# Kernel optimization log

Measured on AMD Instinct MI355X. Metric: run time of the kernel, lower is better.

Reference implementation:

```python
import jax, jax.numpy as jnp
import numpy as np

D_IN = 1024
D_OUT = 1024
NUM_HEADS = 16
HEAD_DIM = D_OUT // NUM_HEADS


def setup_inputs() -> dict:
    key = jax.random.key(0)
    ks = jax.random.split(key, 6)
    s = 0.02
    return {
        "x": jax.random.normal(ks[0], (2, 2048, D_IN), dtype=jnp.float32),
        "Wq": jax.random.normal(ks[1], (D_IN, D_OUT), dtype=jnp.float32) * s,
        "Wk": jax.random.normal(ks[2], (D_IN, D_OUT), dtype=jnp.float32) * s,
        "Wv": jax.random.normal(ks[3], (D_IN, D_OUT), dtype=jnp.float32) * s,
        "Wo": jax.random.normal(ks[4], (D_OUT, D_OUT), dtype=jnp.float32) * s,
        "bo": jax.random.normal(ks[5], (D_OUT,), dtype=jnp.float32) * s,
    }


def reference(x, Wq, Wk, Wv, Wo, bo):
    B, S, d_in = x.shape
    # projections, split into heads: [B, H, S, Dh]
    def split_heads(t):
        return t.reshape(B, S, NUM_HEADS, HEAD_DIM).transpose(0, 2, 1, 3)

    q = split_heads(x @ Wq)
    k = split_heads(x @ Wk)
    v = split_heads(x @ Wv)

    # raw scores [B, H, S, S]
    scores = jnp.einsum("bhqd,bhkd->bhqk", q, k)
    # causal mask applied BEFORE scaling (as in original; -inf unaffected by scale)
    causal = jnp.triu(jnp.ones((S, S), dtype=bool), k=1)
    scores = jnp.where(causal, -jnp.inf, scores)
    # NOTE: original scales by sqrt(d_in) = sqrt(x.shape[-1]), not sqrt(head_dim)
    scores = scores / jnp.sqrt(jnp.asarray(d_in, dtype=scores.dtype))
    weights = jax.nn.softmax(scores, axis=-1)
    # dropout p=0.0 -> identity

    out = jnp.einsum("bhqk,bhkd->bhqd", weights, v)
    out = out.transpose(0, 2, 1, 3).reshape(B, S, D_OUT)
    return out @ Wo + bo
```

## Files before the change

### kernel.cpp

```cpp
#include <hip/hip_runtime.h>

#define D_MODEL 1024
#define SEQ     2048
#define BATCH   2
#define NHEAD   16
#define HDIM    64

typedef __attribute__((ext_vector_type(4))) float  f32x4;
typedef __attribute__((ext_vector_type(8))) __bf16 bf16x8;
typedef __attribute__((ext_vector_type(4))) __bf16 bf16x4;
typedef __attribute__((ext_vector_type(2))) unsigned int u32x2;

__device__ __forceinline__ void gld_lds16(const void* g, void* l) {
  __builtin_amdgcn_global_load_lds(
      (const __attribute__((address_space(1))) void*)g,
      (__attribute__((address_space(3))) void*)l, 16, 0, 0);
}

__global__ void k_convert(const float* __restrict__ in, __bf16* __restrict__ out) {
  int i = blockIdx.x * blockDim.x + threadIdx.x;
  float4 v = ((const float4*)in)[i];
  bf16x4 o;
  o[0] = (__bf16)v.x; o[1] = (__bf16)v.y; o[2] = (__bf16)v.z; o[3] = (__bf16)v.w;
  ((bf16x4*)out)[i] = o;
}

__global__ void k_transw(const float* __restrict__ Wq, const float* __restrict__ Wk,
                         const float* __restrict__ Wv, const float* __restrict__ Wo,
                         __bf16* __restrict__ Wqkvt, __bf16* __restrict__ Wot) {
  __shared__ __bf16 T[64][72];
  const int z = blockIdx.z;
  const float* src = (z==0)?Wq:(z==1)?Wk:(z==2)?Wv:Wo;
  __bf16* dst = (z<3) ? (Wqkvt + (size_t)z*D_MODEL*D_MODEL) : Wot;
  const float scl = (z==0) ? 0.03125f : 1.0f;
  const int k0 = blockIdx.x*64, n0 = blockIdx.y*64;
  const int t = threadIdx.x;
  const int kl = t>>4, nl4 = (t&15)*4;
  #pragma unroll
  for (int part = 0; part < 4; ++part) {
    const int k = part*16 + kl;
    float4 v = *(const float4*)(src + (size_t)(k0+k)*D_MODEL + n0 + nl4);
    T[nl4+0][k] = (__bf16)(v.x*scl);
    T[nl4+1][k] = (__bf16)(v.y*scl);
    T[nl4+2][k] = (__bf16)(v.z*scl);
    T[nl4+3][k] = (__bf16)(v.w*scl);
  }
  __syncthreads();
  const int nl = t>>3, kc = (t&7)*8;
  #pragma unroll
  for (int part = 0; part < 2; ++part) {
    int n = part*32 + nl;
    bf16x8 o = *(const bf16x8*)&T[n][kc];
    *(bf16x8*)(dst + (size_t)(n0+n)*D_MODEL + k0 + kc) = o;
  }
}

template<int OUTF32>
__global__ __launch_bounds__(256)
void k_gemm_bt(const __bf16* __restrict__ A, const __bf16* __restrict__ Bt,
               void* __restrict__ Cv, const float* __restrict__ bias,
               const int K, const int N) {
  __shared__ __bf16 As[128*32];
  __shared__ __bf16 Bs[128*32];
  const int t = threadIdx.x;
  const int w = t>>6, l = t&63;
  const int lr = l&15, g = l>>4;
  const int m0 = blockIdx.y*128, n0 = blockIdx.x*128;
  const int wr = (w>>1)*64, wc = (w&1)*64;
  f32x4 acc[4][4] = {};

  const int srow = w*16 + (l>>2);
  const int sc8  = (l&3)*8;
  const __bf16* Ag = A  + (size_t)(m0 + srow)*K + sc8;
  const __bf16* Bg = Bt + (size_t)(n0 + srow)*K + sc8;
  char* Al = (char*)As + w*1024;
  char* Bl = (char*)Bs + w*1024;

  for (int k0 = 0; k0 < K; k0 += 32) {
    __syncthreads();
    gld_lds16(Ag + k0,                 Al);
    gld_lds16(Ag + (size_t)64*K + k0,  Al + 4096);
    gld_lds16(Bg + k0,                 Bl);
    gld_lds16(Bg + (size_t)64*K + k0,  Bl + 4096);
    __syncthreads();
    bf16x8 af[4], bf[4];
    #pragma unroll
    for (int mi=0;mi<4;++mi)
      af[mi] = *(const bf16x8*)((const char*)As + (wr + mi*16 + lr)*64 + (g<<4));
    #pragma unroll
    for (int ni=0;ni<4;++ni)
      bf[ni] = *(const bf16x8*)((const char*)Bs + (wc + ni*16 + lr)*64 + (g<<4));
    #pragma unroll
    for (int mi=0;mi<4;++mi)
      #pragma unroll
      for (int ni=0;ni<4;++ni)
        acc[mi][ni] = __builtin_amdgcn_mfma_f32_16x16x32_bf16(af[mi], bf[ni], acc[mi][ni], 0, 0, 0);
  }

  if (OUTF32) {
    float* C = (float*)Cv;
    #pragma unroll
    for (int ni=0;ni<4;++ni) {
      const int col = n0 + wc + ni*16 + lr;
      const float bv = bias[col];
      #pragma unroll
      for (int mi=0;mi<4;++mi)
        #pragma unroll
        for (int r=0;r<4;++r) {
          const int row = m0 + wr + mi*16 + g*4 + r;
          C[(size_t)row*N + col] = acc[mi][ni][r] + bv;
        }
    }
  } else {
    __bf16* C = (__bf16*)Cv;
    #pragma unroll
    for (int ni=0;ni<4;++ni) {
      const int col = n0 + wc + ni*16 + lr;
      #pragma unroll
      for (int mi=0;mi<4;++mi)
        #pragma unroll
        for (int r=0;r<4;++r) {
          const int row = m0 + wr + mi*16 + g*4 + r;
          C[(size_t)row*N + col] = (__bf16)acc[mi][ni][r];
        }
    }
  }
}

__global__ __launch_bounds__(256)
void k_attn(const __bf16* __restrict__ QKV, __bf16* __restrict__ AO) {
  __shared__ __bf16 Ks[2][64*64];
  __shared__ __bf16 Vs[2][64*64];
  const int t = threadIdx.x;
  const int w = t>>6, l = t&63;
  const int lr = l&15, g = l>>4;
  const int bh = blockIdx.y, b = bh>>4, h = bh&15;
  const size_t rb = (size_t)b*SEQ;

  const int skey = t>>3, sc = t&7;
  const __bf16* Kg = QKV + rb*3072 + 1024 + h*64 + sc*8;
  const __bf16* Vg = Kg + 1024;
  const int ksw = skey*128 + ((sc ^ (skey&7))<<4);
  const int vsw = ((skey>>4)*4 + (sc>>1))*512 + (skey&15)*32 + (sc&1)*16;

  for (int half = 0; half < 2; ++half) {
    const int qb = (half==0) ? (int)blockIdx.x : 31 - (int)blockIdx.x;
    const int nt = qb + 1;
    const int q0 = qb*64 + w*16;

    bf16x8 qf[2];
    #pragma unroll
    for (int kc=0;kc<2;++kc)
      qf[kc] = *(const bf16x8*)(QKV + (rb + q0 + lr)*3072 + h*64 + kc*32 + g*8);

    f32x4 oacc[4] = {};
    float mrun = -1e30f, lrun = 0.f;

    uint4 kR0 = *(const uint4*)(Kg + (size_t)skey*3072);
    uint4 kR1 = *(const uint4*)(Kg + (size_t)(skey+32)*3072);
    uint4 vR0 = *(const uint4*)(Vg + (size_t)skey*3072);
    uint4 vR1 = *(const uint4*)(Vg + (size_t)(skey+32)*3072);
    __syncthreads();
    {
      char* K0 = (char*)&Ks[0][0]; char* V0 = (char*)&Vs[0][0];
      *(uint4*)(K0 + ksw) = kR0;  *(uint4*)(K0 + ksw + 4096) = kR1;
      *(uint4*)(V0 + vsw) = vR0;  *(uint4*)(V0 + vsw + 4096) = vR1;
    }
    if (nt > 1) {
      kR0 = *(const uint4*)(Kg + (size_t)(64+skey)*3072);
      kR1 = *(const uint4*)(Kg + (size_t)(64+skey+32)*3072);
      vR0 = *(const uint4*)(Vg + (size_t)(64+skey)*3072);
      vR1 = *(const uint4*)(Vg + (size_t)(64+skey+32)*3072);
    }

    int cur = 0;
    for (int kt = 0; kt < nt; ++kt) {
      __syncthreads();
      if (kt+1 < nt) {
        char* Kn = (char*)&Ks[cur^1][0]; char* Vn = (char*)&Vs[cur^1][0];
        *(uint4*)(Kn + ksw) = kR0;  *(uint4*)(Kn + ksw + 4096) = kR1;
        *(uint4*)(Vn + vsw) = vR0;  *(uint4*)(Vn + vsw + 4096) = vR1;
        if (kt+2 < nt) {
          const size_t base = (size_t)(kt+2)*64;
          kR0 = *(const uint4*)(Kg + (base+skey)*3072);
          kR1 = *(const uint4*)(Kg + (base+skey+32)*3072);
          vR0 = *(const uint4*)(Vg + (base+skey)*3072);
          vR1 = *(const uint4*)(Vg + (base+skey+32)*3072);
        }
      }

      const char* Kb = (const char*)&Ks[cur][0];
      f32x4 sa[4] = {};
      #pragma unroll
      for (int kc=0;kc<2;++kc)
        #pragma unroll
        for (int kb=0;kb<4;++kb) {
          bf16x8 kfv = *(const bf16x8*)(Kb + (kb*16+lr)*128 + (((kc*4+g) ^ (lr&7))<<4));
          sa[kb] = __builtin_amdgcn_mfma_f32_16x16x32_bf16(kfv, qf[kc], sa[kb], 0,0,0);
        }

      if (kt == nt-1) {
        const int qg = q0 + lr;
        #pragma unroll
        for (int kb=0;kb<4;++kb)
          #pragma unroll
          for (int r=0;r<4;++r)
            if (kt*64 + kb*16 + 4*g + r > qg) sa[kb][r] = -1e30f;
      }

      float mx = sa[0][0];
      #pragma unroll
      for (int kb=0;kb<4;++kb)
        #pragma unroll
        for (int r=0;r<4;++r) mx = fmaxf(mx, sa[kb][r]);
      mx = fmaxf(mx, __shfl_xor(mx, 16));
      mx = fmaxf(mx, __shfl_xor(mx, 32));
      const float mnew = fmaxf(mrun, mx);
      const float al = __expf(mrun - mnew);
      mrun = mnew;
      float ls = 0.f;
      #pragma unroll
      for (int kb=0;kb<4;++kb)
        #pragma unroll
        for (int r=0;r<4;++r) { float p = __expf(sa[kb][r]-mnew); sa[kb][r] = p; ls += p; }
      ls += __shfl_xor(ls, 16);
      ls += __shfl_xor(ls, 32);
      lrun = lrun*al + ls;
      float alq[4];
      #pragma unroll
      for (int r=0;r<4;++r) alq[r] = __shfl(al, g*4+r);
      #pragma unroll
      for (int nb=0;nb<4;++nb)
        #pragma unroll
        for (int r=0;r<4;++r) oacc[nb][r] *= alq[r];

      const __attribute__((address_space(3))) char* trp =
          (const __attribute__((address_space(3))) char*)((const char*)&Vs[cur][0]) + l*8;
      #pragma unroll
      for (int kc=0;kc<2;++kc) {
        bf16x8 pa;
        #pragma unroll
        for (int j=0;j<4;++j) { pa[j] = (__bf16)sa[2*kc][j]; pa[4+j] = (__bf16)sa[2*kc+1][j]; }
        u32x2 t0[4], t1[4];
        #pragma unroll
        for (int nb=0;nb<4;++nb) {
          asm volatile("ds_read_b64_tr_b16 %0, %1 offset:%2"
                       : "=v"(t0[nb]) : "v"(trp), "i"(((2*kc)*4+nb)*512) : "memory");
          asm volatile("ds_read_b64_tr_b16 %0, %1 offset:%2"
                       : "=v"(t1[nb]) : "v"(trp), "i"(((2*kc+1)*4+nb)*512) : "memory");
        }
        asm volatile("s_waitcnt lgkmcnt(0)" ::: "memory");
        __builtin_amdgcn_sched_barrier(0);
        #pragma unroll
        for (int nb=0;nb<4;++nb) {
          union { u32x2 h[2]; bf16x8 v; } U;
          U.h[0] = t0[nb]; U.h[1] = t1[nb];
          oacc[nb] = __builtin_amdgcn_mfma_f32_16x16x32_bf16(pa, U.v, oacc[nb], 0,0,0);
        }
      }
      cur ^= 1;
    }

    const float rinv = 1.0f / lrun;
    float rq[4];
    #pragma unroll
    for (int r=0;r<4;++r) rq[r] = __shfl(rinv, g*4+r);
    #pragma unroll
    for (int nb=0;nb<4;++nb)
      #pragma unroll
      for (int r=0;r<4;++r)
        AO[(rb + q0 + g*4 + r)*1024 + h*64 + nb*16 + lr] = (__bf16)(oacc[nb][r] * rq[r]);
  }
}

extern "C" void kernel_launch(void* const* d_in, const int* in_sizes, int n_in,
                              void* d_out, int out_size, void* d_ws, size_t ws_size,
                              hipStream_t stream) {
  (void)in_sizes; (void)n_in; (void)out_size; (void)ws_size;
  const float* x  = (const float*)d_in[0];
  const float* Wq = (const float*)d_in[1];
  const float* Wk = (const float*)d_in[2];
  const float* Wv = (const float*)d_in[3];
  const float* Wo = (const float*)d_in[4];
  const float* bo = (const float*)d_in[5];
  float* out = (float*)d_out;
  char* ws = (char*)d_ws;

  __bf16* Xbf   = (__bf16*)(ws);
  __bf16* Wqkvt = (__bf16*)(ws + (size_t)(8<<20));
  __bf16* Wot   = (__bf16*)(ws + (size_t)(14<<20));
  __bf16* QKV   = (__bf16*)(ws + (size_t)(16<<20));
  __bf16* AO    = Xbf;

  k_convert<<<4096, 256, 0, stream>>>(x, Xbf);
  k_transw<<<dim3(16,16,4), 256, 0, stream>>>(Wq, Wk, Wv, Wo, Wqkvt, Wot);
  k_gemm_bt<0><<<dim3(24,32), 256, 0, stream>>>(Xbf, Wqkvt, (void*)QKV, nullptr, 1024, 3072);
  k_attn<<<dim3(16,32), 256, 0, stream>>>(QKV, AO);
  k_gemm_bt<1><<<dim3(8,32), 256, 0, stream>>>(AO, Wot, (void*)out, bo, 1024, 1024);
}
```

Measured before the change: 198.7 us.

## Remap attention to one Q-tile per block, add lazy rescale, narrow output GEMM tile

```diff
diff --git a/kernel.cpp b/kernel.cpp
--- a/kernel.cpp
+++ b/kernel.cpp
@@ -55,19 +55,20 @@
   }
 }
 
-template<int OUTF32>
+template<int OUTF32, int NI>
 __global__ __launch_bounds__(256)
 void k_gemm_bt(const __bf16* __restrict__ A, const __bf16* __restrict__ Bt,
                void* __restrict__ Cv, const float* __restrict__ bias,
                const int K, const int N) {
   __shared__ __bf16 As[128*32];
-  __shared__ __bf16 Bs[128*32];
+  __shared__ __bf16 Bs[NI*32*32];
   const int t = threadIdx.x;
   const int w = t>>6, l = t&63;
   const int lr = l&15, g = l>>4;
-  const int m0 = blockIdx.y*128, n0 = blockIdx.x*128;
-  const int wr = (w>>1)*64, wc = (w&1)*64;
-  f32x4 acc[4][4] = {};
+  const int BN = NI*32;
+  const int m0 = blockIdx.y*128, n0 = blockIdx.x*BN;
+  const int wr = (w>>1)*64, wc = (w&1)*(16*NI);
+  f32x4 acc[4][NI] = {};
 
   const int srow = w*16 + (l>>2);
   const int sc8  = (l&3)*8;
@@ -81,26 +82,27 @@
     gld_lds16(Ag + k0,                 Al);
     gld_lds16(Ag + (size_t)64*K + k0,  Al + 4096);
     gld_lds16(Bg + k0,                 Bl);
-    gld_lds16(Bg + (size_t)64*K + k0,  Bl + 4096);
+    if (NI == 4)
+      gld_lds16(Bg + (size_t)64*K + k0, Bl + 4096);
     __syncthreads();
-    bf16x8 af[4], bf[4];
+    bf16x8 af[4], bf[NI];
     #pragma unroll
     for (int mi=0;mi<4;++mi)
       af[mi] = *(const bf16x8*)((const char*)As + (wr + mi*16 + lr)*64 + (g<<4));
     #pragma unroll
-    for (int ni=0;ni<4;++ni)
+    for (int ni=0;ni<NI;++ni)
       bf[ni] = *(const bf16x8*)((const char*)Bs + (wc + ni*16 + lr)*64 + (g<<4));
     #pragma unroll
     for (int mi=0;mi<4;++mi)
       #pragma unroll
-      for (int ni=0;ni<4;++ni)
+      for (int ni=0;ni<NI;++ni)
         acc[mi][ni] = __builtin_amdgcn_mfma_f32_16x16x32_bf16(af[mi], bf[ni], acc[mi][ni], 0, 0, 0);
   }
 
   if (OUTF32) {
     float* C = (float*)Cv;
     #pragma unroll
-    for (int ni=0;ni<4;++ni) {
+    for (int ni=0;ni<NI;++ni) {
       const int col = n0 + wc + ni*16 + lr;
       const float bv = bias[col];
       #pragma unroll
@@ -114,7 +116,7 @@
   } else {
     __bf16* C = (__bf16*)Cv;
     #pragma unroll
-    for (int ni=0;ni<4;++ni) {
+    for (int ni=0;ni<NI;++ni) {
       const int col = n0 + wc + ni*16 + lr;
       #pragma unroll
       for (int mi=0;mi<4;++mi)
@@ -134,8 +136,15 @@
   const int t = threadIdx.x;
   const int w = t>>6, l = t&63;
   const int lr = l&15, g = l>>4;
-  const int bh = blockIdx.y, b = bh>>4, h = bh&15;
+
+  const int id = blockIdx.x;
+  const int xcd = id & 7, j = id >> 3;
+  const int qb = 31 - (j & 31);
+  const int bh = xcd + 8*(j >> 5);
+  const int b = bh >> 4, h = bh & 15;
   const size_t rb = (size_t)b*SEQ;
+  const int nt = qb + 1;
+  const int q0 = qb*64 + w*16;
 
   const int skey = t>>3, sc = t&7;
   const __bf16* Kg = QKV + rb*3072 + 1024 + h*64 + sc*8;
@@ -143,89 +152,76 @@
   const int ksw = skey*128 + ((sc ^ (skey&7))<<4);
   const int vsw = ((skey>>4)*4 + (sc>>1))*512 + (skey&15)*32 + (sc&1)*16;
 
-  for (int half = 0; half < 2; ++half) {
-    const int qb = (half==0) ? (int)blockIdx.x : 31 - (int)blockIdx.x;
-    const int nt = qb + 1;
-    const int q0 = qb*64 + w*16;
-
-    bf16x8 qf[2];
+  bf16x8 qf[2];
+  #pragma unroll
+  for (int kc=0;kc<2;++kc)
+    qf[kc] = *(const bf16x8*)(QKV + (rb + q0 + lr)*3072 + h*64 + kc*32 + g*8);
+
+  f32x4 oacc[4] = {};
+  float mrun = -1e30f, lrun = 0.f;
+
+  uint4 kR0 = *(const uint4*)(Kg + (size_t)skey*3072);
+  uint4 kR1 = *(const uint4*)(Kg + (size_t)(skey+32)*3072);
+  uint4 vR0 = *(const uint4*)(Vg + (size_t)skey*3072);
+  uint4 vR1 = *(const uint4*)(Vg + (size_t)(skey+32)*3072);
+  {
+    char* K0 = (char*)&Ks[0][0]; char* V0 = (char*)&Vs[0][0];
+    *(uint4*)(K0 + ksw) = kR0;  *(uint4*)(K0 + ksw + 4096) = kR1;
+    *(uint4*)(V0 + vsw) = vR0;  *(uint4*)(V0 + vsw + 4096) = vR1;
+  }
+  if (nt > 1) {
+    kR0 = *(const uint4*)(Kg + (size_t)(64+skey)*3072);
+    kR1 = *(const uint4*)(Kg + (size_t)(64+skey+32)*3072);
+    vR0 = *(const uint4*)(Vg + (size_t)(64+skey)*3072);
+    vR1 = *(const uint4*)(Vg + (size_t)(64+skey+32)*3072);
+  }
+
+  int cur = 0;
+  for (int kt = 0; kt < nt; ++kt) {
+    __syncthreads();
+    if (kt+1 < nt) {
+      char* Kn = (char*)&Ks[cur^1][0]; char* Vn = (char*)&Vs[cur^1][0];
+      *(uint4*)(Kn + ksw) = kR0;  *(uint4*)(Kn + ksw + 4096) = kR1;
+      *(uint4*)(Vn + vsw) = vR0;  *(uint4*)(Vn + vsw + 4096) = vR1;
+      if (kt+2 < nt) {
+        const size_t base = (size_t)(kt+2)*64;
+        kR0 = *(const uint4*)(Kg + (base+skey)*3072);
+        kR1 = *(const uint4*)(Kg + (base+skey+32)*3072);
+        vR0 = *(const uint4*)(Vg + (base+skey)*3072);
+        vR1 = *(const uint4*)(Vg + (base+skey+32)*3072);
+      }
+    }
+
+    const char* Kb = (const char*)&Ks[cur][0];
+    f32x4 sa[4] = {};
     #pragma unroll
     for (int kc=0;kc<2;++kc)
-      qf[kc] = *(const bf16x8*)(QKV + (rb + q0 + lr)*3072 + h*64 + kc*32 + g*8);
-
-    f32x4 oacc[4] = {};
-    float mrun = -1e30f, lrun = 0.f;
-
-    uint4 kR0 = *(const uint4*)(Kg + (size_t)skey*3072);
-    uint4 kR1 = *(const uint4*)(Kg + (size_t)(skey+32)*3072);
-    uint4 vR0 = *(const uint4*)(Vg + (size_t)skey*3072);
-    uint4 vR1 = *(const uint4*)(Vg + (size_t)(skey+32)*3072);
-    __syncthreads();
-    {
-      char* K0 = (char*)&Ks[0][0]; char* V0 = (char*)&Vs[0][0];
-      *(uint4*)(K0 + ksw) = kR0;  *(uint4*)(K0 + ksw + 4096) = kR1;
-      *(uint4*)(V0 + vsw) = vR0;  *(uint4*)(V0 + vsw + 4096) = vR1;
-    }
-    if (nt > 1) {
-      kR0 = *(const uint4*)(Kg + (size_t)(64+skey)*3072);
-      kR1 = *(const uint4*)(Kg + (size_t)(64+skey+32)*3072);
-      vR0 = *(const uint4*)(Vg + (size_t)(64+skey)*3072);
-      vR1 = *(const uint4*)(Vg + (size_t)(64+skey+32)*3072);
-    }
-
-    int cur = 0;
-    for (int kt = 0; kt < nt; ++kt) {
-      __syncthreads();
-      if (kt+1 < nt) {
-        char* Kn = (char*)&Ks[cur^1][0]; char* Vn = (char*)&Vs[cur^1][0];
-        *(uint4*)(Kn + ksw) = kR0;  *(uint4*)(Kn + ksw + 4096) = kR1;
-        *(uint4*)(Vn + vsw) = vR0;  *(uint4*)(Vn + vsw + 4096) = vR1;
-        if (kt+2 < nt) {
-          const size_t base = (size_t)(kt+2)*64;
-          kR0 = *(const uint4*)(Kg + (base+skey)*3072);
-          kR1 = *(const uint4*)(Kg + (base+skey+32)*3072);
-          vR0 = *(const uint4*)(Vg + (base+skey)*3072);
-          vR1 = *(const uint4*)(Vg + (base+skey+32)*3072);
-        }
+      #pragma unroll
+      for (int kb=0;kb<4;++kb) {
+        bf16x8 kfv = *(const bf16x8*)(Kb + (kb*16+lr)*128 + (((kc*4+g) ^ (lr&7))<<4));
+        sa[kb] = __builtin_amdgcn_mfma_f32_16x16x32_bf16(kfv, qf[kc], sa[kb], 0,0,0);
       }
 
-      const char* Kb = (const char*)&Ks[cur][0];
-      f32x4 sa[4] = {};
-      #pragma unroll
-      for (int kc=0;kc<2;++kc)
-        #pragma unroll
-        for (int kb=0;kb<4;++kb) {
-          bf16x8 kfv = *(const bf16x8*)(Kb + (kb*16+lr)*128 + (((kc*4+g) ^ (lr&7))<<4));
-          sa[kb] = __builtin_amdgcn_mfma_f32_16x16x32_bf16(kfv, qf[kc], sa[kb], 0,0,0);
-        }
-
-      if (kt == nt-1) {
-        const int qg = q0 + lr;
-        #pragma unroll
-        for (int kb=0;kb<4;++kb)
-          #pragma unroll
-          for (int r=0;r<4;++r)
-            if (kt*64 + kb*16 + 4*g + r > qg) sa[kb][r] = -1e30f;
-      }
-
-      float mx = sa[0][0];
+    if (kt == nt-1) {
+      const int qg = q0 + lr;
       #pragma unroll
       for (int kb=0;kb<4;++kb)
         #pragma unroll
-        for (int r=0;r<4;++r) mx = fmaxf(mx, sa[kb][r]);
-      mx = fmaxf(mx, __shfl_xor(mx, 16));
-      mx = fmaxf(mx, __shfl_xor(mx, 32));
+        for (int r=0;r<4;++r)
+          if (kt*64 + kb*16 + 4*g + r > qg) sa[kb][r] = -1e30f;
+    }
+
+    float mx = sa[0][0];
+    #pragma unroll
+    for (int kb=0;kb<4;++kb)
+      #pragma unroll
+      for (int r=0;r<4;++r) mx = fmaxf(mx, sa[kb][r]);
+    mx = fmaxf(mx, __shfl_xor(mx, 16));
+    mx = fmaxf(mx, __shfl_xor(mx, 32));
+    if (!__all(mx <= mrun + 8.0f)) {
       const float mnew = fmaxf(mrun, mx);
       const float al = __expf(mrun - mnew);
-      mrun = mnew;
-      float ls = 0.f;
-      #pragma unroll
-      for (int kb=0;kb<4;++kb)
-        #pragma unroll
-        for (int r=0;r<4;++r) { float p = __expf(sa[kb][r]-mnew); sa[kb][r] = p; ls += p; }
-      ls += __shfl_xor(ls, 16);
-      ls += __shfl_xor(ls, 32);
-      lrun = lrun*al + ls;
+      lrun *= al;
       float alq[4];
       #pragma unroll
       for (int r=0;r<4;++r) alq[r] = __shfl(al, g*4+r);
@@ -233,44 +229,53 @@
       for (int nb=0;nb<4;++nb)
         #pragma unroll
         for (int r=0;r<4;++r) oacc[nb][r] *= alq[r];
-
-      const __attribute__((address_space(3))) char* trp =
-          (const __attribute__((address_space(3))) char*)((const char*)&Vs[cur][0]) + l*8;
-      #pragma unroll
-      for (int kc=0;kc<2;++kc) {
-        bf16x8 pa;
-        #pragma unroll
-        for (int j=0;j<4;++j) { pa[j] = (__bf16)sa[2*kc][j]; pa[4+j] = (__bf16)sa[2*kc+1][j]; }
-        u32x2 t0[4], t1[4];
-        #pragma unroll
-        for (int nb=0;nb<4;++nb) {
-          asm volatile("ds_read_b64_tr_b16 %0, %1 offset:%2"
-                       : "=v"(t0[nb]) : "v"(trp), "i"(((2*kc)*4+nb)*512) : "memory");
-          asm volatile("ds_read_b64_tr_b16 %0, %1 offset:%2"
-                       : "=v"(t1[nb]) : "v"(trp), "i"(((2*kc+1)*4+nb)*512) : "memory");
-        }
-        asm volatile("s_waitcnt lgkmcnt(0)" ::: "memory");
-        __builtin_amdgcn_sched_barrier(0);
-        #pragma unroll
-        for (int nb=0;nb<4;++nb) {
-          union { u32x2 h[2]; bf16x8 v; } U;
-          U.h[0] = t0[nb]; U.h[1] = t1[nb];
-          oacc[nb] = __builtin_amdgcn_mfma_f32_16x16x32_bf16(pa, U.v, oacc[nb], 0,0,0);
-        }
+      mrun = mnew;
+    }
+    float ls = 0.f;
+    #pragma unroll
+    for (int kb=0;kb<4;++kb)
+      #pragma unroll
+      for (int r=0;r<4;++r) { float p = __expf(sa[kb][r]-mrun); sa[kb][r] = p; ls += p; }
+    ls += __shfl_xor(ls, 16);
+    ls += __shfl_xor(ls, 32);
+    lrun += ls;
+
+    const __attribute__((address_space(3))) char* trp =
+        (const __attribute__((address_space(3))) char*)((const char*)&Vs[cur][0]) + l*8;
+    #pragma unroll
+    for (int kc=0;kc<2;++kc) {
+      bf16x8 pa;
+      #pragma unroll
+      for (int j2=0;j2<4;++j2) { pa[j2] = (__bf16)sa[2*kc][j2]; pa[4+j2] = (__bf16)sa[2*kc+1][j2]; }
+      u32x2 t0[4], t1[4];
+      #pragma unroll
+      for (int nb=0;nb<4;++nb) {
+        asm volatile("ds_read_b64_tr_b16 %0, %1 offset:%2"
+                     : "=v"(t0[nb]) : "v"(trp), "i"(((2*kc)*4+nb)*512) : "memory");
+        asm volatile("ds_read_b64_tr_b16 %0, %1 offset:%2"
+                     : "=v"(t1[nb]) : "v"(trp), "i"(((2*kc+1)*4+nb)*512) : "memory");
       }
-      cur ^= 1;
-    }
-
-    const float rinv = 1.0f / lrun;
-    float rq[4];
-    #pragma unroll
-    for (int r=0;r<4;++r) rq[r] = __shfl(rinv, g*4+r);
-    #pragma unroll
-    for (int nb=0;nb<4;++nb)
-      #pragma unroll
-      for (int r=0;r<4;++r)
-        AO[(rb + q0 + g*4 + r)*1024 + h*64 + nb*16 + lr] = (__bf16)(oacc[nb][r] * rq[r]);
-  }
+      asm volatile("s_waitcnt lgkmcnt(0)" ::: "memory");
+      __builtin_amdgcn_sched_barrier(0);
+      #pragma unroll
+      for (int nb=0;nb<4;++nb) {
+        union { u32x2 h[2]; bf16x8 v; } U;
+        U.h[0] = t0[nb]; U.h[1] = t1[nb];
+        oacc[nb] = __builtin_amdgcn_mfma_f32_16x16x32_bf16(pa, U.v, oacc[nb], 0,0,0);
+      }
+    }
+    cur ^= 1;
+  }
+
+  const float rinv = 1.0f / lrun;
+  float rq[4];
+  #pragma unroll
+  for (int r=0;r<4;++r) rq[r] = __shfl(rinv, g*4+r);
+  #pragma unroll
+  for (int nb=0;nb<4;++nb)
+    #pragma unroll
+    for (int r=0;r<4;++r)
+      AO[(rb + q0 + g*4 + r)*1024 + h*64 + nb*16 + lr] = (__bf16)(oacc[nb][r] * rq[r]);
 }
 
 extern "C" void kernel_launch(void* const* d_in, const int* in_sizes, int n_in,
@@ -294,7 +299,7 @@
 
   k_convert<<<4096, 256, 0, stream>>>(x, Xbf);
   k_transw<<<dim3(16,16,4), 256, 0, stream>>>(Wq, Wk, Wv, Wo, Wqkvt, Wot);
-  k_gemm_bt<0><<<dim3(24,32), 256, 0, stream>>>(Xbf, Wqkvt, (void*)QKV, nullptr, 1024, 3072);
-  k_attn<<<dim3(16,32), 256, 0, stream>>>(QKV, AO);
-  k_gemm_bt<1><<<dim3(8,32), 256, 0, stream>>>(AO, Wot, (void*)out, bo, 1024, 1024);
-}
+  k_gemm_bt<0,4><<<dim3(24,32), 256, 0, stream>>>(Xbf, Wqkvt, (void*)QKV, nullptr, 1024, 3072);
+  k_attn<<<1024, 256, 0, stream>>>(QKV, AO);
+  k_gemm_bt<1,2><<<dim3(16,32), 256, 0, stream>>>(AO, Wot, (void*)out, bo, 1024, 1024);
+}
```

Measured after the change: 207.8 us. +4.6%, slower.
